# Optimization experiments

Hardware: AMD Instinct MI355X
Metric: run time of the kernel (lower is better)

## Reference

```python
import jax, jax.numpy as jnp
import numpy as np

D_MODEL = 1024
N_HEADS = 16
D_KEYS = 64
GROUP_POSITIONS = [list(range(g * 32, (g + 1) * 32)) for g in range(4)]


def _make_tables(group_positions, dim):
    # InGroup table: pe[j,i] = (j/Lg) * L0 / 10000^(2*(i//2)/dim)
    L0 = len(group_positions[0])
    rows = []
    for grp in group_positions:
        Lg = len(grp)
        for j in range(Lg):
            rows.append([j / Lg * L0 / np.power(10000.0, 2 * (i // 2) / dim) for i in range(dim)])
    pe = np.array(rows)
    ingroup = np.concatenate([np.sin(pe[:, 0::2]), np.cos(pe[:, 1::2])], axis=1).astype(np.float32)
    # Sequence (group) table: pe[j,i] = grp[0] / 10000^(j/Lg), constant over i
    rows = []
    for grp in group_positions:
        Lg = len(grp)
        for j in range(Lg):
            rows.append([grp[0] / np.power(10000.0, j / Lg) for _ in range(dim)])
    pe = np.array(rows)
    seq = np.concatenate([np.sin(pe[:, 0::2]), np.cos(pe[:, 1::2])], axis=1).astype(np.float32)
    return jnp.asarray(ingroup), jnp.asarray(seq)


def setup_inputs() -> dict:
    key = jax.random.key(0)
    ks = jax.random.split(key, 12)
    B, L, S = 64, 128, 128
    dqk = D_KEYS * N_HEADS
    sc_in = 1.0 / np.sqrt(D_MODEL)
    sc_out = 1.0 / np.sqrt(dqk)
    inp = {
        "queries": jax.random.normal(ks[0], (B, L, D_MODEL), jnp.float32),
        "keys": jax.random.normal(ks[1], (B, S, D_MODEL), jnp.float32),
        "values": jax.random.normal(ks[2], (B, S, D_MODEL), jnp.float32),
        "attn_mask": jnp.zeros((B, 1, L, S), dtype=bool),
        "Wq": jax.random.normal(ks[3], (D_MODEL, dqk), jnp.float32) * sc_in,
        "bq": jnp.zeros((dqk,), jnp.float32),
        "Wk": jax.random.normal(ks[4], (D_MODEL, dqk), jnp.float32) * sc_in,
        "bk": jnp.zeros((dqk,), jnp.float32),
        "Wv": jax.random.normal(ks[5], (D_MODEL, dqk), jnp.float32) * sc_in,
        "bv": jnp.zeros((dqk,), jnp.float32),
        "Wo": jax.random.normal(ks[6], (dqk, D_MODEL), jnp.float32) * sc_out,
        "bo": jnp.zeros((D_MODEL,), jnp.float32),
    }
    pos_ingroup, pos_seq = _make_tables(GROUP_POSITIONS, D_KEYS)
    inp["pos_ingroup"] = pos_ingroup  # [n_pos, d_keys]
    inp["pos_seq"] = pos_seq          # [n_pos, d_keys]
    return inp


def _rope(x, pos):
    # x: [B, H, L, D]; pos: [L, D]
    sin, cos = jnp.split(pos, 2, axis=-1)
    sin_pos = jnp.stack([sin, sin], axis=-1).reshape(pos.shape)
    cos_pos = jnp.stack([cos, cos], axis=-1).reshape(pos.shape)
    rot = jnp.stack([-x[..., 1::2], x[..., ::2]], axis=-1).reshape(x.shape)
    return x * cos_pos + rot * sin_pos


def reference(queries, keys, values, attn_mask, Wq, bq, Wk, bk, Wv, bv, Wo, bo, pos_ingroup, pos_seq):
    B, L, _ = queries.shape
    S = keys.shape[1]
    H, E = N_HEADS, D_KEYS
    q = (queries @ Wq + bq).reshape(B, L, H, E).transpose(0, 2, 1, 3)  # [B,H,L,E]
    k = (keys @ Wk + bk).reshape(B, S, H, E).transpose(0, 2, 1, 3)
    v = (values @ Wv + bv).reshape(B, S, H, E).transpose(0, 2, 1, 3)
    # group-sequence in-group RoPE, then group RoPE (tables gathered at arange positions)
    q = _rope(_rope(q, pos_ingroup[:L]), pos_seq[:L])
    k = _rope(_rope(k, pos_ingroup[:S]), pos_seq[:S])
    # inner full attention on [B,L,H,E] layout
    scale = 1.0 / jnp.sqrt(jnp.asarray(E, q.dtype))
    scores = jnp.einsum("bhle,bhse->bhls", q, k) * scale
    scores = jnp.where(attn_mask, jnp.asarray(-jnp.inf, scores.dtype), scores)
    attn = jax.nn.softmax(scores, axis=-1)  # [B,H,L,S]
    out = jnp.einsum("bhls,bhsd->blhd", attn, v).reshape(B, L, H * E)
    return out @ Wo + bo, attn
```

## Files before the change

### kernel.cpp

```cpp
#include <hip/hip_runtime.h>
#include <cstdint>

typedef float f32x4 __attribute__((ext_vector_type(4)));
typedef __bf16 bf16x8 __attribute__((ext_vector_type(8)));
typedef unsigned short u16x8 __attribute__((ext_vector_type(8)));

typedef __attribute__((address_space(3))) uint32_t lds_u32;
typedef __attribute__((address_space(1))) const uint32_t glb_u32;

#define GLOAD_LDS16(gp, lp) \
  __builtin_amdgcn_global_load_lds((glb_u32*)(uintptr_t)(gp), (lds_u32*)(uintptr_t)(lp), 16, 0, 0)

__device__ inline unsigned short f2bf(float f) {
  union { float f; uint32_t u; } v; v.f = f;
  uint32_t u = v.u;
  return (unsigned short)((u + 0x7fffu + ((u >> 16) & 1u)) >> 16);
}

__global__ void prep_all(const float* __restrict__ q, const float* __restrict__ k,
                         const float* __restrict__ v,
                         const float* __restrict__ wq, const float* __restrict__ wk,
                         const float* __restrict__ wv, const float* __restrict__ wo,
                         const float* __restrict__ ing, const float* __restrict__ seq,
                         unsigned short* __restrict__ dst, unsigned short* __restrict__ wt,
                         float* __restrict__ cosc, float* __restrict__ sinc)
{
  __shared__ float t[64][65];
  const int bx = blockIdx.x;
  const int tid = threadIdx.x;

  if (bx < 24576) {
    int z = bx >> 13;
    int b8 = bx & 8191;
    const float* src = (z == 0) ? q : (z == 1) ? k : v;
    unsigned short* d = dst + (size_t)z * 8388608;
    size_t i = ((size_t)b8 * 256 + tid) * 4;
    float4 f = *(const float4*)&src[i];
    ushort4 o;
    o.x = f2bf(f.x); o.y = f2bf(f.y); o.z = f2bf(f.z); o.w = f2bf(f.w);
    *(ushort4*)&d[i] = o;
  } else if (bx < 25600) {
    int pb = bx - 24576;
    int z = pb >> 8;
    int rem = pb & 255;
    const float* W = (z == 0) ? wq : (z == 1) ? wk : (z == 2) ? wv : wo;
    unsigned short* Wt = wt + (size_t)z * 1048576;
    const int n0 = (rem & 15) * 64, k0 = (rem >> 4) * 64;
    const int tx = tid & 63, ty = tid >> 6;
#pragma unroll
    for (int i = 0; i < 16; i++) {
      int row = i * 4 + ty;
      t[row][tx] = W[(size_t)(k0 + row) * 1024 + n0 + tx];
    }
    __syncthreads();
#pragma unroll
    for (int i = 0; i < 16; i++) {
      int row = i * 4 + ty;
      Wt[(size_t)(n0 + row) * 1024 + k0 + tx] = f2bf(t[tx][row]);
    }
  } else {
    int idx = (bx - 25600) * 256 + tid;
    int j = idx >> 5, i = idx & 31;
    float s1 = ing[j * 64 + i], c1 = ing[j * 64 + 32 + i];
    float s2 = seq[j * 64 + i], c2 = seq[j * 64 + 32 + i];
    cosc[idx] = c1 * c2 - s1 * s2;
    sinc[idx] = s1 * c2 + c1 * s2;
  }
}

__global__ __launch_bounds__(256, 2)
void gemm_bt(const unsigned short* __restrict__ Abase,
             const unsigned short* __restrict__ Bbase,
             const float* __restrict__ b0, const float* __restrict__ b1,
             const float* __restrict__ b2,
             unsigned short* __restrict__ qb, unsigned short* __restrict__ kb,
             unsigned short* __restrict__ vtb,
             float* __restrict__ outf,
             const float* __restrict__ cosc, const float* __restrict__ sinc,
             int final_mode)
{
  __shared__ __attribute__((aligned(16))) unsigned short Sh[2][8192];
  unsigned short* As = &Sh[0][0];
  unsigned short* Bs = &Sh[1][0];

  const int tid = threadIdx.x;
  const int lane = tid & 63;
  const int wave = tid >> 6;
  const int quad = lane >> 4;
  const int l15 = lane & 15;

  const int z = blockIdx.z;
  const int tileM = blockIdx.x * 128;
  const int tileN = blockIdx.y * 128;
  const int K = 1024;

  const unsigned short* A = Abase + (size_t)z * (8192u * 1024u);
  const unsigned short* B = Bbase + (size_t)z * (1024u * 1024u);

  const int wm = (wave >> 1) * 64;
  const int wn = (wave & 1) * 64;

  f32x4 acc[4][4];
#pragma unroll
  for (int a = 0; a < 4; a++)
#pragma unroll
    for (int n = 0; n < 4; n++)
      acc[a][n] = (f32x4){0.f, 0.f, 0.f, 0.f};

  for (int k0 = 0; k0 < K; k0 += 64) {
#pragma unroll
    for (int cc = 0; cc < 4; cc++) {
      int c = wave * 4 + cc;
      int s = c * 64 + lane;
      int row = s >> 3;
      int gc = (s & 7) ^ (row & 7);
      const unsigned short* ga = A + (size_t)(tileM + row) * K + k0 + gc * 8;
      const unsigned short* gb = B + (size_t)(tileN + row) * K + k0 + gc * 8;
      GLOAD_LDS16(ga, &As[c * 512]);
      GLOAD_LDS16(gb, &Bs[c * 512]);
    }
    __syncthreads();

#pragma unroll
    for (int ks = 0; ks < 2; ks++) {
      bf16x8 af[4], bfr[4];
#pragma unroll
      for (int a = 0; a < 4; a++) {
        int r = wm + a * 16 + l15;
        int cp = (ks * 4 + quad) ^ (r & 7);
        af[a] = *(const bf16x8*)&As[(r * 8 + cp) * 8];
      }
#pragma unroll
      for (int n = 0; n < 4; n++) {
        int r = wn + n * 16 + l15;
        int cp = (ks * 4 + quad) ^ (r & 7);
        bfr[n] = *(const bf16x8*)&Bs[(r * 8 + cp) * 8];
      }
#pragma unroll
      for (int a = 0; a < 4; a++)
#pragma unroll
        for (int n = 0; n < 4; n++)
          acc[a][n] = __builtin_amdgcn_mfma_f32_16x16x32_bf16(af[a], bfr[n], acc[a][n], 0, 0, 0);
    }
    __syncthreads();
  }

  if (final_mode) {
    float* flatf = (float*)&Sh[0][0];
#pragma unroll
    for (int h = 0; h < 2; h++) {
      __syncthreads();
      if ((wave >> 1) == h) {
#pragma unroll
        for (int n = 0; n < 4; n++) {
          int lcg = wn + n * 16 + l15;
          float bias = b0[tileN + lcg];
#pragma unroll
          for (int a = 0; a < 4; a++)
#pragma unroll
            for (int reg = 0; reg < 4; reg++) {
              int lrow = a * 16 + quad * 4 + reg;
              flatf[lrow * 128 + lcg] = acc[a][n][reg] + bias;
            }
        }
      }
      __syncthreads();
#pragma unroll
      for (int c = 0; c < 8; c++) {
        int ff = (c * 256 + tid) * 4;
        int row = ff >> 7, col = ff & 127;
        *(f32x4*)&outf[(size_t)(tileM + h * 64 + row) * 1024 + tileN + col] =
            *(const f32x4*)&flatf[ff];
      }
    }
  } else {
    const float* bias = (z == 0) ? b0 : (z == 1) ? b1 : b2;
    unsigned short* outq = (z == 0) ? qb : kb;
    unsigned short* flat = &Sh[0][0];

#pragma unroll
    for (int n = 0; n < 4; n++) {
      int lcg = wn + n * 16 + l15;
      float bv_ = bias[tileN + lcg];
      int e = lcg & 63;
#pragma unroll
      for (int a = 0; a < 4; a++)
#pragma unroll
        for (int reg = 0; reg < 4; reg++) {
          int l = wm + a * 16 + quad * 4 + reg;
          float v = acc[a][n][reg] + bv_;
          unsigned short ov;
          int f;
          if (z == 2) {
            ov = f2bf(v);
            f = lcg * 128 + l;
            f ^= ((f >> 7) & 15) << 3;
          } else {
            float other = __shfl_xor(v, 1);
            float cs = cosc[l * 32 + (e >> 1)];
            float sn = sinc[l * 32 + (e >> 1)];
            ov = f2bf(v * cs + ((e & 1) ? other : -other) * sn);
            f = ((lcg >> 6) << 13) + (l << 6) + e;
            f ^= ((f >> 8) & 7) << 4;
          }
          flat[f] = ov;
        }
    }
    __syncthreads();

    unsigned short* gout = ((z == 2) ? vtb : outq) +
                           ((size_t)(tileM >> 7) * 16 + (tileN >> 6)) * 8192;
#pragma unroll
    for (int c = 0; c < 8; c++) {
      int f0 = tid * 64 + c * 8;
      int s0 = (z == 2) ? (f0 ^ (((f0 >> 7) & 15) << 3))
                        : (f0 ^ (((f0 >> 8) & 7) << 4));
      *(u16x8*)&gout[f0] = *(const u16x8*)&flat[s0];
    }
  }
}

__global__ __launch_bounds__(256, 2)
void attn_kernel(const unsigned short* __restrict__ qb,
                 const unsigned short* __restrict__ kb,
                 const unsigned short* __restrict__ vtb,
                 const unsigned char* __restrict__ mask,
                 float* __restrict__ attn_out,
                 unsigned short* __restrict__ ob)
{
  __shared__ __attribute__((aligned(16))) unsigned short Pb[128 * 136];
  const int tid = threadIdx.x;
  const int lane = tid & 63;
  const int wave = tid >> 6;
  const int quad = lane >> 4;
  const int l15 = lane & 15;
  const int bh = blockIdx.x;
  const int b = bh >> 4;
  const int h = bh & 15;

  const unsigned short* q = qb + (size_t)bh * 128 * 64;
  const unsigned short* k = kb + (size_t)bh * 128 * 64;
  const unsigned short* vt = vtb + (size_t)bh * 64 * 128;

  f32x4 sacc[2][8];
#pragma unroll
  for (int mt = 0; mt < 2; mt++)
#pragma unroll
    for (int nt = 0; nt < 8; nt++)
      sacc[mt][nt] = (f32x4){0.f, 0.f, 0.f, 0.f};

#pragma unroll
  for (int ks = 0; ks < 2; ks++) {
    bf16x8 aq[2], bk[8];
#pragma unroll
    for (int mt = 0; mt < 2; mt++)
      aq[mt] = *(const bf16x8*)&q[(size_t)(wave * 32 + mt * 16 + l15) * 64 + ks * 32 + quad * 8];
#pragma unroll
    for (int nt = 0; nt < 8; nt++)
      bk[nt] = *(const bf16x8*)&k[(size_t)(nt * 16 + l15) * 64 + ks * 32 + quad * 8];
#pragma unroll
    for (int mt = 0; mt < 2; mt++)
#pragma unroll
      for (int nt = 0; nt < 8; nt++)
        sacc[mt][nt] = __builtin_amdgcn_mfma_f32_16x16x32_bf16(aq[mt], bk[nt], sacc[mt][nt], 0, 0, 0);
  }

  const float scale = 0.125f;
#pragma unroll
  for (int mt = 0; mt < 2; mt++) {
#pragma unroll
    for (int reg = 0; reg < 4; reg++) {
      int r = wave * 32 + mt * 16 + quad * 4 + reg;
      const unsigned char* mrow = mask + ((size_t)b * 128 + r) * 128;
      float sv[8];
#pragma unroll
      for (int nt = 0; nt < 8; nt++) {
        float x = sacc[mt][nt][reg] * scale;
        if (mrow[nt * 16 + l15]) x = -__builtin_inff();
        sv[nt] = x;
      }
      float m = sv[0];
#pragma unroll
      for (int nt = 1; nt < 8; nt++) m = fmaxf(m, sv[nt]);
#pragma unroll
      for (int off = 1; off < 16; off <<= 1) m = fmaxf(m, __shfl_xor(m, off));
      float s = 0.f;
#pragma unroll
      for (int nt = 0; nt < 8; nt++) { sv[nt] = __expf(sv[nt] - m); s += sv[nt]; }
#pragma unroll
      for (int off = 1; off < 16; off <<= 1) s += __shfl_xor(s, off);
      float inv = 1.0f / s;
      float* arow = attn_out + ((size_t)bh * 128 + r) * 128;
#pragma unroll
      for (int nt = 0; nt < 8; nt++) {
        float p = sv[nt] * inv;
        arow[nt * 16 + l15] = p;
        Pb[r * 136 + nt * 16 + l15] = f2bf(p);
      }
    }
  }
  __syncthreads();

  f32x4 oacc[2][4];
#pragma unroll
  for (int mt = 0; mt < 2; mt++)
#pragma unroll
    for (int nt = 0; nt < 4; nt++)
      oacc[mt][nt] = (f32x4){0.f, 0.f, 0.f, 0.f};

#pragma unroll
  for (int ks = 0; ks < 4; ks++) {
    bf16x8 bv[4], ap[2];
#pragma unroll
    for (int nt = 0; nt < 4; nt++)
      bv[nt] = *(const bf16x8*)&vt[(size_t)(nt * 16 + l15) * 128 + ks * 32 + quad * 8];
#pragma unroll
    for (int mt = 0; mt < 2; mt++)
      ap[mt] = *(const bf16x8*)&Pb[(size_t)(wave * 32 + mt * 16 + l15) * 136 + ks * 32 + quad * 8];
#pragma unroll
    for (int mt = 0; mt < 2; mt++)
#pragma unroll
      for (int nt = 0; nt < 4; nt++)
        oacc[mt][nt] = __builtin_amdgcn_mfma_f32_16x16x32_bf16(ap[mt], bv[nt], oacc[mt][nt], 0, 0, 0);
  }

#pragma unroll
  for (int mt = 0; mt < 2; mt++)
#pragma unroll
    for (int nt = 0; nt < 4; nt++)
#pragma unroll
      for (int reg = 0; reg < 4; reg++) {
        int r = wave * 32 + mt * 16 + quad * 4 + reg;
        int e = nt * 16 + l15;
        ob[((size_t)b * 128 + r) * 1024 + h * 64 + e] = f2bf(oacc[mt][nt][reg]);
      }
}

extern "C" void kernel_launch(void* const* d_in, const int* in_sizes, int n_in,
                              void* d_out, int out_size, void* d_ws, size_t ws_size,
                              hipStream_t stream)
{
  const float* queries = (const float*)d_in[0];
  const float* keys    = (const float*)d_in[1];
  const float* values  = (const float*)d_in[2];
  const unsigned char* mask = (const unsigned char*)d_in[3];
  const float* Wq = (const float*)d_in[4];
  const float* bq = (const float*)d_in[5];
  const float* Wk = (const float*)d_in[6];
  const float* bk = (const float*)d_in[7];
  const float* Wv = (const float*)d_in[8];
  const float* bv = (const float*)d_in[9];
  const float* Wo = (const float*)d_in[10];
  const float* bo = (const float*)d_in[11];
  const float* ping = (const float*)d_in[12];
  const float* pseq = (const float*)d_in[13];

  float* out  = (float*)d_out;
  float* attn = out + 8388608;
  unsigned short* Xbf = (unsigned short*)attn;

  char* ws = (char*)d_ws;
  unsigned short* Wt  = (unsigned short*)(ws);
  float* cosc = (float*)(ws + 8388608);
  float* sinc = (float*)(ws + 8388608 + 16384);
  unsigned short* qbuf = (unsigned short*)(ws + 8421376);
  unsigned short* kbuf = (unsigned short*)(ws + 8421376 + 16777216);
  unsigned short* vtbuf= (unsigned short*)(ws + 8421376 + 2*16777216);
  unsigned short* obuf = (unsigned short*)(ws + 8421376 + 3*16777216);

  prep_all<<<dim3(25616), 256, 0, stream>>>(queries, keys, values,
                                            Wq, Wk, Wv, Wo, ping, pseq,
                                            Xbf, Wt, cosc, sinc);
  gemm_bt<<<dim3(64, 8, 3), 256, 0, stream>>>(Xbf, Wt, bq, bk, bv,
                                              qbuf, kbuf, vtbuf, nullptr,
                                              cosc, sinc, 0);
  attn_kernel<<<dim3(1024), 256, 0, stream>>>(qbuf, kbuf, vtbuf, mask, attn, obuf);
  gemm_bt<<<dim3(64, 8, 1), 256, 0, stream>>>(obuf, Wt + 3 * 1048576, bo, bo, bo,
                                              qbuf, kbuf, vtbuf, out,
                                              cosc, sinc, 1);
}
```

Measured before the change: 338.8 us.

## Bit-pack attention mask and stage attn-prob stores through LDS for coalescing

The bool mask is packed into 16-bit words during the prep kernel, so the attention kernel reads one 16-byte vector per row instead of scattered byte loads. The fp32 attention probabilities are first buffered in a new LDS tile, one half of the rows at a time, and then written to global memory as contiguous 16-byte vectors instead of strided 4-byte scalar stores. The cost is extra prep work, a larger LDS footprint that may reduce occupancy, and two more barrier pairs in the attention kernel.

```diff
diff --git a/kernel.cpp b/kernel.cpp
--- a/kernel.cpp
+++ b/kernel.cpp
@@ -22,8 +22,10 @@
                          const float* __restrict__ wq, const float* __restrict__ wk,
                          const float* __restrict__ wv, const float* __restrict__ wo,
                          const float* __restrict__ ing, const float* __restrict__ seq,
+                         const unsigned char* __restrict__ mask,
                          unsigned short* __restrict__ dst, unsigned short* __restrict__ wt,
-                         float* __restrict__ cosc, float* __restrict__ sinc)
+                         float* __restrict__ cosc, float* __restrict__ sinc,
+                         unsigned short* __restrict__ pmask)
 {
   __shared__ float t[64][65];
   const int bx = blockIdx.x;
@@ -58,13 +60,26 @@
       int row = i * 4 + ty;
       Wt[(size_t)(n0 + row) * 1024 + k0 + tx] = f2bf(t[tx][row]);
     }
-  } else {
+  } else if (bx < 25616) {
     int idx = (bx - 25600) * 256 + tid;
     int j = idx >> 5, i = idx & 31;
     float s1 = ing[j * 64 + i], c1 = ing[j * 64 + 32 + i];
     float s2 = seq[j * 64 + i], c2 = seq[j * 64 + 32 + i];
     cosc[idx] = c1 * c2 - s1 * s2;
     sinc[idx] = s1 * c2 + c1 * s2;
+  } else {
+    int ci = (bx - 25616) * 256 + tid;
+    uint4 mv = *(const uint4*)(mask + (size_t)ci * 16);
+    const uint32_t* mw = (const uint32_t*)&mv;
+    unsigned out = 0;
+#pragma unroll
+    for (int w = 0; w < 4; w++) {
+      uint32_t x = mw[w];
+#pragma unroll
+      for (int kk = 0; kk < 4; kk++)
+        out |= (((x >> (8 * kk)) & 0xffu) ? 1u : 0u) << (w * 4 + kk);
+    }
+    pmask[ci] = (unsigned short)out;
   }
 }
 
@@ -224,11 +239,12 @@
 void attn_kernel(const unsigned short* __restrict__ qb,
                  const unsigned short* __restrict__ kb,
                  const unsigned short* __restrict__ vtb,
-                 const unsigned char* __restrict__ mask,
+                 const unsigned short* __restrict__ pmask,
                  float* __restrict__ attn_out,
                  unsigned short* __restrict__ ob)
 {
   __shared__ __attribute__((aligned(16))) unsigned short Pb[128 * 136];
+  __shared__ __attribute__((aligned(16))) float Pf[64 * 132];
   const int tid = threadIdx.x;
   const int lane = tid & 63;
   const int wave = tid >> 6;
@@ -266,17 +282,19 @@
   }
 
   const float scale = 0.125f;
+  float pv[2][4][8];
 #pragma unroll
   for (int mt = 0; mt < 2; mt++) {
 #pragma unroll
     for (int reg = 0; reg < 4; reg++) {
       int r = wave * 32 + mt * 16 + quad * 4 + reg;
-      const unsigned char* mrow = mask + ((size_t)b * 128 + r) * 128;
+      uint4 pm = *(const uint4*)&pmask[((size_t)b * 128 + r) * 8];
+      const uint32_t* pw = (const uint32_t*)&pm;
       float sv[8];
 #pragma unroll
       for (int nt = 0; nt < 8; nt++) {
         float x = sacc[mt][nt][reg] * scale;
-        if (mrow[nt * 16 + l15]) x = -__builtin_inff();
+        if ((pw[nt >> 1] >> ((nt & 1) * 16 + l15)) & 1u) x = -__builtin_inff();
         sv[nt] = x;
       }
       float m = sv[0];
@@ -290,16 +308,38 @@
 #pragma unroll
       for (int off = 1; off < 16; off <<= 1) s += __shfl_xor(s, off);
       float inv = 1.0f / s;
-      float* arow = attn_out + ((size_t)bh * 128 + r) * 128;
 #pragma unroll
       for (int nt = 0; nt < 8; nt++) {
         float p = sv[nt] * inv;
-        arow[nt * 16 + l15] = p;
+        pv[mt][reg][nt] = p;
         Pb[r * 136 + nt * 16 + l15] = f2bf(p);
       }
     }
   }
-  __syncthreads();
+
+#pragma unroll
+  for (int hh = 0; hh < 2; hh++) {
+    __syncthreads();
+    if ((wave >> 1) == hh) {
+#pragma unroll
+      for (int mt = 0; mt < 2; mt++)
+#pragma unroll
+        for (int reg = 0; reg < 4; reg++) {
+          int lr = (wave & 1) * 32 + mt * 16 + quad * 4 + reg;
+#pragma unroll
+          for (int nt = 0; nt < 8; nt++)
+            Pf[lr * 132 + nt * 16 + l15] = pv[mt][reg][nt];
+        }
+    }
+    __syncthreads();
+    float* abase = attn_out + (size_t)bh * 16384 + hh * 8192;
+#pragma unroll
+    for (int c = 0; c < 8; c++) {
+      int ff = (c * 256 + tid) * 4;
+      int row = ff >> 7, col = ff & 127;
+      *(f32x4*)&abase[row * 128 + col] = *(const f32x4*)&Pf[row * 132 + col];
+    }
+  }
 
   f32x4 oacc[2][4];
 #pragma unroll
@@ -363,18 +403,19 @@
   unsigned short* Wt  = (unsigned short*)(ws);
   float* cosc = (float*)(ws + 8388608);
   float* sinc = (float*)(ws + 8388608 + 16384);
-  unsigned short* qbuf = (unsigned short*)(ws + 8421376);
-  unsigned short* kbuf = (unsigned short*)(ws + 8421376 + 16777216);
-  unsigned short* vtbuf= (unsigned short*)(ws + 8421376 + 2*16777216);
-  unsigned short* obuf = (unsigned short*)(ws + 8421376 + 3*16777216);
-
-  prep_all<<<dim3(25616), 256, 0, stream>>>(queries, keys, values,
-                                            Wq, Wk, Wv, Wo, ping, pseq,
-                                            Xbf, Wt, cosc, sinc);
+  unsigned short* pmask= (unsigned short*)(ws + 8388608 + 32768);
+  unsigned short* qbuf = (unsigned short*)(ws + 8552448);
+  unsigned short* kbuf = (unsigned short*)(ws + 8552448 + 16777216);
+  unsigned short* vtbuf= (unsigned short*)(ws + 8552448 + 2*16777216);
+  unsigned short* obuf = (unsigned short*)(ws + 8552448 + 3*16777216);
+
+  prep_all<<<dim3(25872), 256, 0, stream>>>(queries, keys, values,
+                                            Wq, Wk, Wv, Wo, ping, pseq, mask,
+                                            Xbf, Wt, cosc, sinc, pmask);
   gemm_bt<<<dim3(64, 8, 3), 256, 0, stream>>>(Xbf, Wt, bq, bk, bv,
                                               qbuf, kbuf, vtbuf, nullptr,
                                               cosc, sinc, 0);
-  attn_kernel<<<dim3(1024), 256, 0, stream>>>(qbuf, kbuf, vtbuf, mask, attn, obuf);
+  attn_kernel<<<dim3(1024), 256, 0, stream>>>(qbuf, kbuf, vtbuf, pmask, attn, obuf);
   gemm_bt<<<dim3(64, 8, 1), 256, 0, stream>>>(obuf, Wt + 3 * 1048576, bo, bo, bo,
                                               qbuf, kbuf, vtbuf, out,
                                               cosc, sinc, 1);
```

After: 339.8 us. No clear change (+0.3%).
